# Optimization experiments

Hardware: AMD Instinct MI355X
Metric: run time of the kernel (lower is better)

The kernel has to match this reference:

```python
import jax, jax.numpy as jnp
import numpy as np

B, S, E = 4, 2048, 1024
H, D = 16, 64  # num_heads, attention_head_dim


def setup_inputs() -> dict:
    key = jax.random.key(0)
    ks = jax.random.split(key, 9)
    scale_e = 1.0 / np.sqrt(E)
    scale_hd = 1.0 / np.sqrt(H * D)
    x = jax.random.normal(ks[0], (B, S, E), dtype=jnp.float32)
    # per-head projection weights, stacked: [H, E, D]
    Wq = jax.random.uniform(ks[1], (H, E, D), minval=-scale_e, maxval=scale_e, dtype=jnp.float32)
    Wk = jax.random.uniform(ks[2], (H, E, D), minval=-scale_e, maxval=scale_e, dtype=jnp.float32)
    Wv = jax.random.uniform(ks[3], (H, E, D), minval=-scale_e, maxval=scale_e, dtype=jnp.float32)
    bq = jax.random.uniform(ks[4], (H, D), minval=-scale_e, maxval=scale_e, dtype=jnp.float32)
    bk = jax.random.uniform(ks[5], (H, D), minval=-scale_e, maxval=scale_e, dtype=jnp.float32)
    bv = jax.random.uniform(ks[6], (H, D), minval=-scale_e, maxval=scale_e, dtype=jnp.float32)
    Wo = jax.random.uniform(ks[7], (H * D, E), minval=-scale_hd, maxval=scale_hd, dtype=jnp.float32)
    bo = jax.random.uniform(ks[8], (E,), minval=-scale_hd, maxval=scale_hd, dtype=jnp.float32)
    return {"x": x, "Wq": Wq, "Wk": Wk, "Wv": Wv, "bq": bq, "bk": bk, "bv": bv, "Wo": Wo, "bo": bo}


def reference(x, Wq, Wk, Wv, bq, bk, bv, Wo, bo):
    # Per-head QKV projections, vectorized over heads: [B,H,S,D]
    Q = jnp.einsum('bse,hed->bhsd', x, Wq) + bq[None, :, None, :]
    K = jnp.einsum('bse,hed->bhsd', x, Wk) + bk[None, :, None, :]
    V = jnp.einsum('bse,hed->bhsd', x, Wv) + bv[None, :, None, :]
    scale = 1.0 / jnp.sqrt(jnp.asarray(D, dtype=Q.dtype))
    scores = jnp.einsum('bhsd,bhtd->bhst', Q, K) * scale  # [B,H,S,S]
    attn = jax.nn.softmax(scores, axis=-1)
    Z = jnp.einsum('bhst,bhtd->bhsd', attn, V)            # [B,H,S,D]
    # concat heads on feature dim -> [B,S,H*D], then output projection
    Zc = jnp.transpose(Z, (0, 2, 1, 3)).reshape(B, S, H * D)
    return Zc @ Wo + bo
```

## Files before the change

kernel.cpp:

```cpp
#include <hip/hip_runtime.h>


typedef __attribute__((ext_vector_type(4)))  float   f32x4;
typedef __attribute__((ext_vector_type(16))) float   f32x16;
typedef __attribute__((ext_vector_type(8)))  __bf16  bf16x8;
typedef __attribute__((ext_vector_type(4)))  __bf16  bf16x4;
typedef __attribute__((ext_vector_type(4)))  unsigned int u32x4;
typedef unsigned int u32;

#if __has_builtin(__builtin_amdgcn_exp2f)
#define EXP2F(x) __builtin_amdgcn_exp2f(x)
#else
#define EXP2F(x) exp2f(x)
#endif

__device__ __forceinline__ f32x4 fzero4() {
    f32x4 z = {0.f, 0.f, 0.f, 0.f};
    return z;
}
__device__ __forceinline__ f32x16 fzero16() {
    f32x16 z;
#pragma unroll
    for (int i = 0; i < 16; i++) z[i] = 0.f;
    return z;
}

__device__ __forceinline__ u32 cvtpk_bf16(float lo, float hi_) {
    u32 r;
    asm("v_cvt_pk_bf16_f32 %0, %1, %2" : "=v"(r) : "v"(lo), "v"(hi_));
    return r;
}

__device__ __forceinline__ void gload_lds16(const void* g, void* l) {
    __builtin_amdgcn_global_load_lds(
        (const __attribute__((address_space(1))) u32*)g,
        (__attribute__((address_space(3))) u32*)l, 16, 0, 0);
}

__global__ __launch_bounds__(256) void prep(
    const float* __restrict__ x,  __bf16* __restrict__ xb,
    const float* __restrict__ Wq, const float* __restrict__ Wk,
    const float* __restrict__ Wv, const float* __restrict__ Wo,
    __bf16* __restrict__ Wqkv, __bf16* __restrict__ Wot,
    const float* __restrict__ bq, const float* __restrict__ bk,
    const float* __restrict__ bv, float* __restrict__ bqkv) {
    __shared__ float t[32][33];
    const int tid = threadIdx.x;
    int bid = blockIdx.x;

    if (bid < 8192) {
        long i = ((long)bid * 256 + tid) * 4;
        float4 v = *(const float4*)(x + i);
        bf16x4 o = { (__bf16)v.x, (__bf16)v.y, (__bf16)v.z, (__bf16)v.w };
        *(bf16x4*)(xb + i) = o;
        return;
    }
    bid -= 8192;
    if (bid < 4096) {
        const float* src;
        __bf16* dst;
        int C, r0, c0;
        if (bid < 3072) {
            const int g = bid >> 10, rem = bid & 1023;
            const float* W = (g == 0) ? Wq : (g == 1) ? Wk : Wv;
            const int z = rem >> 6, bx = rem & 31, by = (rem >> 5) & 1;
            C = 64;
            src = W + (size_t)z * 1024 * 64;
            dst = Wqkv + (size_t)g * 1024 * 1024 + (size_t)z * 1024 * 64;
            r0 = bx * 32; c0 = by * 32;
        } else {
            const int rem = bid - 3072;
            const int bx = rem & 31, by = rem >> 5;
            C = 1024;
            src = Wo; dst = Wot;
            r0 = bx * 32; c0 = by * 32;
        }
        const int xx = tid & 31, yy = tid >> 5;
#pragma unroll
        for (int i = 0; i < 4; i++)
            t[yy + i * 8][xx] = src[(size_t)(r0 + yy + i * 8) * C + c0 + xx];
        __syncthreads();
#pragma unroll
        for (int i = 0; i < 4; i++)
            dst[(size_t)(c0 + yy + i * 8) * 1024 + r0 + xx] =
                (__bf16)t[xx][yy + i * 8];
        return;
    }
    const int n = (bid - 4096) * 256 + tid;
    if (n < 3072) {
        const int tt = n >> 10, r = n & 1023;
        const float* s = (tt == 0) ? bq : (tt == 1) ? bk : bv;
        bqkv[n] = s[r];
    }
}

#define GEMM_STAGE(BUF, KOFF)                                                  \
  {                                                                            \
    gload_lds16(A + arow0 * K + (KOFF) + kcol,                                 \
                (char*)As + (BUF) * 16384 + wid * 1024);                       \
    gload_lds16(A + arow1 * K + (KOFF) + kcol,                                 \
                (char*)As + (BUF) * 16384 + 8192 + wid * 1024);                \
    gload_lds16(Bt + brow * K + (KOFF) + kcol,                                 \
                (char*)Bs + (BUF) * 8192 + wid * 1024);                        \
  }

#define GEMM_COMPUTE(BUF)                                                      \
  {                                                                            \
    bf16x8 a[4], b[4];                                                         \
    _Pragma("unroll")                                                          \
    for (int mi = 0; mi < 4; mi++)                                             \
      a[mi] = *(const bf16x8*)&As[(BUF) * 8192 +                               \
                                  (mr * 64 + mi * 16 + l15) * 32 + l4 * 8];    \
    _Pragma("unroll")                                                          \
    for (int ni = 0; ni < 4; ni++)                                             \
      b[ni] = *(const bf16x8*)&Bs[(BUF) * 4096 +                               \
                                  (nc * 64 + ni * 16 + l15) * 32 + l4 * 8];    \
    _Pragma("unroll")                                                          \
    for (int mi = 0; mi < 4; mi++)                                             \
      _Pragma("unroll")                                                        \
      for (int ni = 0; ni < 4; ni++)                                           \
        acc[mi][ni] = __builtin_amdgcn_mfma_f32_16x16x32_bf16(                 \
            a[mi], b[ni], acc[mi][ni], 0, 0, 0);                               \
  }

#define GEMM_PREAMBLE                                                          \
    const int tid  = threadIdx.x;                                              \
    const int lane = tid & 63, wid = tid >> 6;                                 \
    const int mr = wid >> 1, nc = wid & 1;                                     \
    const int l15 = lane & 15, l4 = lane >> 4;                                 \
    const int bn = blockIdx.x, bm = blockIdx.y;                                \
    const long arow0 = (long)bm * 256 + (tid >> 2);                            \
    const long arow1 = arow0 + 128;                                            \
    const long brow  = (long)bn * 128 + (tid >> 2);                            \
    const int  kcol  = (tid & 3) * 8;                                          \
    f32x4 acc[4][4];                                                           \
    _Pragma("unroll")                                                          \
    for (int i = 0; i < 4; i++)                                                \
      _Pragma("unroll")                                                        \
      for (int j = 0; j < 4; j++) acc[i][j] = fzero4();                        \
    GEMM_STAGE(0, 0)                                                           \
    __syncthreads();                                                           \
    int cur = 0;                                                               \
    for (int k0 = 0; k0 < K; k0 += 32, cur ^= 1) {                             \
        if (k0 + 32 < K) GEMM_STAGE(cur ^ 1, k0 + 32)                          \
        GEMM_COMPUTE(cur)                                                      \
        __syncthreads();                                                       \
    }

template <bool F32OUT>
__global__ __launch_bounds__(512) void gemm_bt(
    const __bf16* __restrict__ A, const __bf16* __restrict__ Bt,
    const float* __restrict__ bias, void* __restrict__ Cout,
    int M, int N, int K, int ldc) {
    __shared__ __bf16 As[2 * 256 * 32];
    __shared__ __bf16 Bs[2 * 128 * 32];
    GEMM_PREAMBLE

#pragma unroll
    for (int mi = 0; mi < 4; mi++)
#pragma unroll
        for (int ni = 0; ni < 4; ni++) {
            const int row = bm * 256 + mr * 64 + mi * 16 + l4 * 4;
            const int col = bn * 128 + nc * 64 + ni * 16 + l15;
            const float bv = bias ? bias[col] : 0.f;
#pragma unroll
            for (int r = 0; r < 4; r++) {
                float v = acc[mi][ni][r] + bv;
                if (F32OUT)
                    ((float*)Cout)[(long)(row + r) * ldc + col] = v;
                else
                    ((__bf16*)Cout)[(long)(row + r) * ldc + col] = (__bf16)v;
            }
        }
}

__global__ __launch_bounds__(512) void gemm_qkv(
    const __bf16* __restrict__ A, const __bf16* __restrict__ Bt,
    const float* __restrict__ bias, __bf16* __restrict__ QKV,
    __bf16* __restrict__ VT, int K) {
    __shared__ __bf16 As[2 * 256 * 32];
    __shared__ __bf16 Bs[2 * 128 * 32];
    GEMM_PREAMBLE

    if (bn < 16) {
#pragma unroll
        for (int mi = 0; mi < 4; mi++)
#pragma unroll
            for (int ni = 0; ni < 4; ni++) {
                const int row = bm * 256 + mr * 64 + mi * 16 + l4 * 4;
                const int col = bn * 128 + nc * 64 + ni * 16 + l15;
                const float bv = bias[col];
#pragma unroll
                for (int r = 0; r < 4; r++)
                    QKV[(long)(row + r) * 3072 + col] =
                        (__bf16)(acc[mi][ni][r] + bv);
            }
    } else {
#pragma unroll
        for (int mi = 0; mi < 4; mi++)
#pragma unroll
            for (int ni = 0; ni < 4; ni++) {
                const int row = bm * 256 + mr * 64 + mi * 16 + l4 * 4;
                const int col = bn * 128 + nc * 64 + ni * 16 + l15;
                const float bv = bias[col];
                const int vcol = col - 2048;
                const int h = vcol >> 6, dcol = vcol & 63;
                const int bb = row >> 11, s = row & 2047;
                bf16x4 o;
#pragma unroll
                for (int r = 0; r < 4; r++)
                    o[r] = (__bf16)(acc[mi][ni][r] + bv);
                *(bf16x4*)&VT[((size_t)(bb * 16 + h) * 64 + dcol) * 2048 + s] = o;
            }
    }
}

#define ATTN_SM_PV(S0, S1, M_R, L_R, O0, O1)                                   \
  {                                                                            \
    float mm[16];                                                              \
    _Pragma("unroll")                                                          \
    for (int i = 0; i < 16; i++) mm[i] = fmaxf(S0[i], S1[i]);                  \
    _Pragma("unroll")                                                          \
    for (int st = 8; st >= 1; st >>= 1)                                        \
      _Pragma("unroll")                                                        \
      for (int i = 0; i < st; i++) mm[i] = fmaxf(mm[i], mm[i + st]);           \
    const float pm = fmaxf(mm[0], __shfl_xor(mm[0], 32));                      \
    if (!__all(pm - M_R <= 64.f)) {              \
      const float mnew = fmaxf(M_R, pm);                                       \
      const float alpha = EXP2F((M_R - mnew) * csc);                           \
      M_R = mnew;                                                              \
      L_R *= alpha;                                                            \
      _Pragma("unroll")                                                        \
      for (int i = 0; i < 16; i++) { O0[i] *= alpha; O1[i] *= alpha; }         \
    }                                                                          \
    const float mc = M_R * csc;                                                \
    float ss[16];                                                              \
    _Pragma("unroll")                                                          \
    for (int i = 0; i < 16; i++) {                                             \
      float p0 = EXP2F(S0[i] * csc - mc); S0[i] = p0;                          \
      float p1 = EXP2F(S1[i] * csc - mc); S1[i] = p1;                          \
      ss[i] = p0 + p1;                                                         \
    }                                                                          \
    _Pragma("unroll")                                                          \
    for (int st = 8; st >= 1; st >>= 1)                                        \
      _Pragma("unroll")                                                        \
      for (int i = 0; i < st; i++) ss[i] += ss[i + st];                        \
    L_R += ss[0] + __shfl_xor(ss[0], 32);                                      \
    __builtin_amdgcn_s_setprio(1);                                             \
    _Pragma("unroll")                                                          \
    for (int kkt = 0; kkt < 4; kkt++) {                                        \
      const int r0 = (kkt & 1) * 8;                                            \
      u32 w0, w1, w2, w3;                                                      \
      if (kkt < 2) {                                                           \
        w0 = cvtpk_bf16(S0[r0],     S0[r0 + 1]);                               \
        w1 = cvtpk_bf16(S0[r0 + 2], S0[r0 + 3]);                               \
        w2 = cvtpk_bf16(S0[r0 + 4], S0[r0 + 5]);                               \
        w3 = cvtpk_bf16(S0[r0 + 6], S0[r0 + 7]);                               \
      } else {                                                                 \
        w0 = cvtpk_bf16(S1[r0],     S1[r0 + 1]);                               \
        w1 = cvtpk_bf16(S1[r0 + 2], S1[r0 + 3]);                               \
        w2 = cvtpk_bf16(S1[r0 + 4], S1[r0 + 5]);                               \
        w3 = cvtpk_bf16(S1[r0 + 6], S1[r0 + 7]);                               \
      }                                                                        \
      asm("v_permlane32_swap_b32 %0, %1" : "+v"(w0), "+v"(w2));                \
      asm("v_permlane32_swap_b32 %0, %1" : "+v"(w1), "+v"(w3));                \
      u32x4 pw = {w0, w1, w2, w3};                                             \
      bf16x8 pf = __builtin_bit_cast(bf16x8, pw);                              \
      O0 = __builtin_amdgcn_mfma_f32_32x32x16_bf16(vf[kkt],     pf, O0, 0, 0, 0); \
      O1 = __builtin_amdgcn_mfma_f32_32x32x16_bf16(vf[4 + kkt], pf, O1, 0, 0, 0); \
    }                                                                          \
    __builtin_amdgcn_s_setprio(0);                                             \
  }

#define ATTN_EPI(O0, O1, L_R, ROWBASE)                                         \
  {                                                                            \
    const float inv = 1.0f / L_R;                                              \
    _Pragma("unroll")                                                          \
    for (int g = 0; g < 4; g++) {                                              \
      bf16x4 t4a, t4b;                                                         \
      _Pragma("unroll")                                                        \
      for (int j = 0; j < 4; j++) {                                            \
        t4a[j] = (__bf16)(O0[4 * g + j] * inv);                                \
        t4b[j] = (__bf16)(O1[4 * g + j] * inv);                                \
      }                                                                        \
      *(bf16x4*)&Tl[trow][g * 8 + hi * 4]      = t4a;                          \
      *(bf16x4*)&Tl[trow][32 + g * 8 + hi * 4] = t4b;                          \
    }                                                                          \
    asm volatile("s_waitcnt lgkmcnt(0)" ::: "memory");                         \
    __builtin_amdgcn_sched_barrier(0);                                         \
    _Pragma("unroll")                                                          \
    for (int i = 0; i < 4; i++) {                                              \
      bf16x8 z = *(const bf16x8*)&Tl[rr][ch + i * 8];                          \
      *(bf16x8*)&Z[((size_t)b * S + (ROWBASE) + rr) * 1024 + h * 64 +          \
                   ch + i * 8] = z;                                            \
    }                                                                          \
    asm volatile("s_waitcnt lgkmcnt(0)" ::: "memory");                         \
    __builtin_amdgcn_sched_barrier(0);                                         \
  }

__global__ __launch_bounds__(256, 2) void attn_fwd(
    const __bf16* __restrict__ QKV, const __bf16* __restrict__ VT,
    __bf16* __restrict__ Z) {
    const int S = 2048, LDQ = 3072;
    const int dd = blockIdx.x;
    const int blk = (dd & 7) * 64 + (dd >> 3);
    const int qt = blk & 7, bh = blk >> 3, b = bh >> 4, h = bh & 15;
    const int tid = threadIdx.x, wid = tid >> 6, lane = tid & 63;
    const int l31 = lane & 31, hi = lane >> 5;

    __shared__ __bf16 smem[16384];

    const __bf16* Qb = QKV + (size_t)b * S * LDQ + h * 64;
    const __bf16* Kb = Qb + 1024;
    const __bf16* Vb = VT + (size_t)bh * 64 * S;
    const int qrowA = qt * 256 + wid * 32;
    const int qrowB = qrowA + 128;

    bf16x8 qfA[4], qfB[4];
#pragma unroll
    for (int kk = 0; kk < 4; kk++) {
        qfA[kk] = *(const bf16x8*)(Qb + (size_t)(qrowA + l31) * LDQ + kk * 16 + hi * 8);
        qfB[kk] = *(const bf16x8*)(Qb + (size_t)(qrowB + l31) * LDQ + kk * 16 + hi * 8);
    }

    const int f0 = wid * 2, f1 = wid * 2 + 1;
    const int kr0 = (f0 >> 2) * 32 + l31, kc0 = (f0 & 3) * 16 + hi * 8;
    const int kr1 = (f1 >> 2) * 32 + l31, kc1 = (f1 & 3) * 16 + hi * 8;
    const int vr0 = kr0, vs0 = kc0;
    const int vr1 = kr1, vs1 = kc1;
    const int ldst = lane * 16;

    f32x16 oA0 = fzero16(), oA1 = fzero16();
    f32x16 oB0 = fzero16(), oB1 = fzero16();
    float m_rA = -1e30f, l_rA = 0.f, m_rB = -1e30f, l_rB = 0.f;
    const float csc = 0.18033688011f;

    gload_lds16(Kb + (size_t)kr0 * LDQ + kc0, (char*)smem + f0 * 1024 + ldst);
    gload_lds16(Kb + (size_t)kr1 * LDQ + kc1, (char*)smem + f1 * 1024 + ldst);
    gload_lds16(Vb + (size_t)vr0 * S + vs0,   (char*)smem + 16384 + f0 * 1024 + ldst);
    gload_lds16(Vb + (size_t)vr1 * S + vs1,   (char*)smem + 16384 + f1 * 1024 + ldst);
    asm volatile("s_waitcnt vmcnt(0)" ::: "memory");
    __syncthreads();

    int cur = 0;
    for (int t0 = 0; t0 < S; t0 += 64, cur ^= 1) {
        if (t0 + 64 < S) {
            char* kl = (char*)smem + (cur ^ 1) * 8192;
            char* vl = (char*)smem + 16384 + (cur ^ 1) * 8192;
            gload_lds16(Kb + (size_t)(t0 + 64 + kr0) * LDQ + kc0, kl + f0 * 1024 + ldst);
            gload_lds16(Kb + (size_t)(t0 + 64 + kr1) * LDQ + kc1, kl + f1 * 1024 + ldst);
            gload_lds16(Vb + (size_t)vr0 * S + t0 + 64 + vs0,     vl + f0 * 1024 + ldst);
            gload_lds16(Vb + (size_t)vr1 * S + t0 + 64 + vs1,     vl + f1 * 1024 + ldst);
        }
        const char* kbase = (const char*)smem + cur * 8192;
        const char* vbase = (const char*)smem + 16384 + cur * 8192;

        bf16x8 kf[8];
#pragma unroll
        for (int f = 0; f < 8; f++)
            kf[f] = *(const bf16x8*)(kbase + f * 1024 + ldst);
        f32x16 sA0 = fzero16(), sA1 = fzero16();
        f32x16 sB0 = fzero16(), sB1 = fzero16();
        __builtin_amdgcn_s_setprio(1);
#pragma unroll
        for (int kk = 0; kk < 4; kk++) {
            sA0 = __builtin_amdgcn_mfma_f32_32x32x16_bf16(kf[kk],     qfA[kk], sA0, 0, 0, 0);
            sA1 = __builtin_amdgcn_mfma_f32_32x32x16_bf16(kf[4 + kk], qfA[kk], sA1, 0, 0, 0);
        }
#pragma unroll
        for (int kk = 0; kk < 4; kk++) {
            sB0 = __builtin_amdgcn_mfma_f32_32x32x16_bf16(kf[kk],     qfB[kk], sB0, 0, 0, 0);
            sB1 = __builtin_amdgcn_mfma_f32_32x32x16_bf16(kf[4 + kk], qfB[kk], sB1, 0, 0, 0);
        }
        __builtin_amdgcn_s_setprio(0);

        bf16x8 vf[8];
#pragma unroll
        for (int f = 0; f < 8; f++)
            vf[f] = *(const bf16x8*)(vbase + f * 1024 + ldst);

        ATTN_SM_PV(sA0, sA1, m_rA, l_rA, oA0, oA1)
        ATTN_SM_PV(sB0, sB1, m_rB, l_rB, oB0, oB1)

        asm volatile("s_waitcnt vmcnt(0)" ::: "memory");
        __syncthreads();
    }

    __bf16 (*Tl)[72] = (__bf16 (*)[72])smem;
    const int trow = wid * 32 + l31;
    const int rr = wid * 32 + (lane >> 1);
    const int ch = (lane & 1) * 32;
    ATTN_EPI(oA0, oA1, l_rA, qt * 256)
    ATTN_EPI(oB0, oB1, l_rB, qt * 256 + 128)
}

extern "C" void kernel_launch(void* const* d_in, const int* in_sizes, int n_in,
                              void* d_out, int out_size, void* d_ws, size_t ws_size,
                              hipStream_t stream) {
    const float* x  = (const float*)d_in[0];
    const float* Wq = (const float*)d_in[1];
    const float* Wk = (const float*)d_in[2];
    const float* Wv = (const float*)d_in[3];
    const float* bq = (const float*)d_in[4];
    const float* bk = (const float*)d_in[5];
    const float* bv = (const float*)d_in[6];
    const float* Wo = (const float*)d_in[7];
    const float* bo = (const float*)d_in[8];
    float* out = (float*)d_out;

    char* p = (char*)d_ws;
    __bf16* xb   = (__bf16*)p; p += 8192L * 1024 * 2;
    __bf16* Wqkv = (__bf16*)p; p += 3072L * 1024 * 2;
    float*  bqkv = (float*)p;  p += 3072L * 4;
    __bf16* QKV  = (__bf16*)p; p += 8192L * 3072 * 2;
    __bf16* VTb  = (__bf16*)p; p += 64L * 64 * 2048 * 2;
    __bf16* Zb   = (__bf16*)p; p += 8192L * 1024 * 2;
    __bf16* Wot  = (__bf16*)p; p += 1024L * 1024 * 2;

    prep<<<12300, 256, 0, stream>>>(x, xb, Wq, Wk, Wv, Wo, Wqkv, Wot,
                                    bq, bk, bv, bqkv);

    gemm_qkv<<<dim3(24, 32), 512, 0, stream>>>(xb, Wqkv, bqkv, QKV, VTb, 1024);
    attn_fwd<<<512, 256, 0, stream>>>(QKV, VTb, Zb);
    gemm_bt<true><<<dim3(8, 32), 512, 0, stream>>>(Zb, Wot, bo, out,
                                                   8192, 1024, 1024, 1024);
}
```

Measured before the change: 211.8 us.

## Pipeline GEMM mainloop with three-stage LDS ring and interleaved phased MFMA

Replaces the double-buffered K=32 GEMM mainloop with a three-deep LDS ring that holds K=64 per stage. It issues the global-to-LDS loads for stage t+2 interleaved between four MFMA sub-phases, waits with explicit vmcnt counts and a single barrier per iteration, and raises wave priority around the MFMA bursts. The aim is to hide global load latency and cut barrier overhead in the QKV and output-projection GEMMs. In exchange, LDS use per block grows to 144KB, which may limit occupancy, and correctness now depends on the hand-counted vmcnt(6) matching the loads actually issued.

Measured after the change: 232.2 us. 9.6% more time.

```diff
diff --git a/kernel.cpp b/kernel.cpp
--- a/kernel.cpp
+++ b/kernel.cpp
@@ -94,57 +94,75 @@
     }
 }
 
-#define GEMM_STAGE(BUF, KOFF)                                                  \
+#define G8_STAGE_A(RING, KOFF, KC, HALF)                                       \
+    gload_lds16(A + (arow0 + (HALF) * 128) * (size_t)K + (KOFF) + (KC) * 32 + acol, \
+                (char*)As + ((RING) * 2 + (KC)) * 16384 + (HALF) * 8192 + tid * 16);
+
+#define G8_STAGE_B(RING, KOFF, KC)                                             \
+    gload_lds16(Bt + (size_t)brow * K + (KOFF) + (KC) * 32 + bcol,             \
+                (char*)Bs + ((RING) * 2 + (KC)) * 8192 + tid * 16);
+
+#define G8_PHASE(RING, MH, NH)                                                 \
   {                                                                            \
-    gload_lds16(A + arow0 * K + (KOFF) + kcol,                                 \
-                (char*)As + (BUF) * 16384 + wid * 1024);                       \
-    gload_lds16(A + arow1 * K + (KOFF) + kcol,                                 \
-                (char*)As + (BUF) * 16384 + 8192 + wid * 1024);                \
-    gload_lds16(Bt + brow * K + (KOFF) + kcol,                                 \
-                (char*)Bs + (BUF) * 8192 + wid * 1024);                        \
+    bf16x8 a0[2], a1[2], b0[2], b1[2];                                         \
+    _Pragma("unroll")                                                          \
+    for (int kc = 0; kc < 2; kc++) {                                           \
+      const char* ab = (const char*)As + ((RING) * 2 + kc) * 16384;            \
+      const char* bb = (const char*)Bs + ((RING) * 2 + kc) * 8192;             \
+      a0[kc] = *(const bf16x8*)(ab + ((mr * 64 + ((MH) * 2 + 0) * 16 + l15) * 32 + l4 * 8) * 2); \
+      a1[kc] = *(const bf16x8*)(ab + ((mr * 64 + ((MH) * 2 + 1) * 16 + l15) * 32 + l4 * 8) * 2); \
+      b0[kc] = *(const bf16x8*)(bb + ((nc * 64 + ((NH) * 2 + 0) * 16 + l15) * 32 + l4 * 8) * 2); \
+      b1[kc] = *(const bf16x8*)(bb + ((nc * 64 + ((NH) * 2 + 1) * 16 + l15) * 32 + l4 * 8) * 2); \
+    }                                                                          \
+    __builtin_amdgcn_s_setprio(1);                                             \
+    _Pragma("unroll")                                                          \
+    for (int kc = 0; kc < 2; kc++) {                                           \
+      acc[(MH)*2+0][(NH)*2+0] = __builtin_amdgcn_mfma_f32_16x16x32_bf16(a0[kc], b0[kc], acc[(MH)*2+0][(NH)*2+0], 0, 0, 0); \
+      acc[(MH)*2+0][(NH)*2+1] = __builtin_amdgcn_mfma_f32_16x16x32_bf16(a0[kc], b1[kc], acc[(MH)*2+0][(NH)*2+1], 0, 0, 0); \
+      acc[(MH)*2+1][(NH)*2+0] = __builtin_amdgcn_mfma_f32_16x16x32_bf16(a1[kc], b0[kc], acc[(MH)*2+1][(NH)*2+0], 0, 0, 0); \
+      acc[(MH)*2+1][(NH)*2+1] = __builtin_amdgcn_mfma_f32_16x16x32_bf16(a1[kc], b1[kc], acc[(MH)*2+1][(NH)*2+1], 0, 0, 0); \
+    }                                                                          \
+    __builtin_amdgcn_s_setprio(0);                                             \
   }
 
-#define GEMM_COMPUTE(BUF)                                                      \
-  {                                                                            \
-    bf16x8 a[4], b[4];                                                         \
-    _Pragma("unroll")                                                          \
-    for (int mi = 0; mi < 4; mi++)                                             \
-      a[mi] = *(const bf16x8*)&As[(BUF) * 8192 +                               \
-                                  (mr * 64 + mi * 16 + l15) * 32 + l4 * 8];    \
-    _Pragma("unroll")                                                          \
-    for (int ni = 0; ni < 4; ni++)                                             \
-      b[ni] = *(const bf16x8*)&Bs[(BUF) * 4096 +                               \
-                                  (nc * 64 + ni * 16 + l15) * 32 + l4 * 8];    \
-    _Pragma("unroll")                                                          \
-    for (int mi = 0; mi < 4; mi++)                                             \
-      _Pragma("unroll")                                                        \
-      for (int ni = 0; ni < 4; ni++)                                           \
-        acc[mi][ni] = __builtin_amdgcn_mfma_f32_16x16x32_bf16(                 \
-            a[mi], b[ni], acc[mi][ni], 0, 0, 0);                               \
-  }
-
-#define GEMM_PREAMBLE                                                          \
+#define G8_PREAMBLE                                                            \
     const int tid  = threadIdx.x;                                              \
     const int lane = tid & 63, wid = tid >> 6;                                 \
     const int mr = wid >> 1, nc = wid & 1;                                     \
     const int l15 = lane & 15, l4 = lane >> 4;                                 \
     const int bn = blockIdx.x, bm = blockIdx.y;                                \
     const long arow0 = (long)bm * 256 + (tid >> 2);                            \
-    const long arow1 = arow0 + 128;                                            \
     const long brow  = (long)bn * 128 + (tid >> 2);                            \
-    const int  kcol  = (tid & 3) * 8;                                          \
+    const int  acol  = (tid & 3) * 8, bcol = (tid & 3) * 8;                    \
     f32x4 acc[4][4];                                                           \
     _Pragma("unroll")                                                          \
     for (int i = 0; i < 4; i++)                                                \
       _Pragma("unroll")                                                        \
-      for (int j = 0; j < 4; j++) acc[i][j] = fzero4();                        \
-    GEMM_STAGE(0, 0)                                                           \
-    __syncthreads();                                                           \
-    int cur = 0;                                                               \
-    for (int k0 = 0; k0 < K; k0 += 32, cur ^= 1) {                             \
-        if (k0 + 32 < K) GEMM_STAGE(cur ^ 1, k0 + 32)                          \
-        GEMM_COMPUTE(cur)                                                      \
-        __syncthreads();                                                       \
+      for (int j = 0; j < 4; j++) acc[i][j] = fzero4();
+
+#define G8_LOOP                                                                \
+    const int NT = K >> 6;                                                     \
+    G8_STAGE_A(0, 0, 0, 0) G8_STAGE_A(0, 0, 0, 1)                              \
+    G8_STAGE_A(0, 0, 1, 0) G8_STAGE_A(0, 0, 1, 1)                              \
+    G8_STAGE_B(0, 0, 0)    G8_STAGE_B(0, 0, 1)                                 \
+    G8_STAGE_A(1, 64, 0, 0) G8_STAGE_A(1, 64, 0, 1)                            \
+    G8_STAGE_A(1, 64, 1, 0) G8_STAGE_A(1, 64, 1, 1)                            \
+    G8_STAGE_B(1, 64, 0)    G8_STAGE_B(1, 64, 1)                               \
+    for (int t = 0; t < NT; ++t) {                                             \
+        const int k0 = t << 6;                                                 \
+        if (t == NT - 1) { asm volatile("s_waitcnt vmcnt(0)" ::: "memory"); }  \
+        else             { asm volatile("s_waitcnt vmcnt(6)" ::: "memory"); }  \
+        __builtin_amdgcn_s_barrier();                                          \
+        const int rg = t % 3;                                                  \
+        const int rs = (t + 2) % 3;                                            \
+        const bool dstg = (t + 2) < NT;                                        \
+        if (dstg) { G8_STAGE_A(rs, k0 + 128, 0, 0) G8_STAGE_A(rs, k0 + 128, 0, 1) } \
+        G8_PHASE(rg, 0, 0)                                                     \
+        if (dstg) { G8_STAGE_A(rs, k0 + 128, 1, 0) G8_STAGE_A(rs, k0 + 128, 1, 1) } \
+        G8_PHASE(rg, 0, 1)                                                     \
+        if (dstg) { G8_STAGE_B(rs, k0 + 128, 0)    G8_STAGE_B(rs, k0 + 128, 1) } \
+        G8_PHASE(rg, 1, 0)                                                     \
+        G8_PHASE(rg, 1, 1)                                                     \
     }
 
 template <bool F32OUT>
@@ -152,9 +170,10 @@
     const __bf16* __restrict__ A, const __bf16* __restrict__ Bt,
     const float* __restrict__ bias, void* __restrict__ Cout,
     int M, int N, int K, int ldc) {
-    __shared__ __bf16 As[2 * 256 * 32];
-    __shared__ __bf16 Bs[2 * 128 * 32];
-    GEMM_PREAMBLE
+    __shared__ __bf16 As[3 * 2 * 8192];
+    __shared__ __bf16 Bs[3 * 2 * 4096];
+    G8_PREAMBLE
+    G8_LOOP
 
 #pragma unroll
     for (int mi = 0; mi < 4; mi++)
@@ -178,9 +197,10 @@
     const __bf16* __restrict__ A, const __bf16* __restrict__ Bt,
     const float* __restrict__ bias, __bf16* __restrict__ QKV,
     __bf16* __restrict__ VT, int K) {
-    __shared__ __bf16 As[2 * 256 * 32];
-    __shared__ __bf16 Bs[2 * 128 * 32];
-    GEMM_PREAMBLE
+    __shared__ __bf16 As[3 * 2 * 8192];
+    __shared__ __bf16 Bs[3 * 2 * 4096];
+    G8_PREAMBLE
+    G8_LOOP
 
     if (bn < 16) {
 #pragma unroll
```
